# Performance work log

Hardware: AMD Instinct MI355X
Metric: run time of the kernel (lower is better)

The kernel has to match this reference:

```python
import jax, jax.numpy as jnp
import numpy as np

N_EMBD = 768

def setup_inputs() -> dict:
    key = jax.random.key(0)
    k1, k2, k3, k4 = jax.random.split(key, 4)
    B, T, head_size = 16, 1024, 128
    x = jax.random.normal(k1, (B, T, N_EMBD), dtype=jnp.float32)
    # nn.Linear(in, out, bias=False): weight stored as (out, in); we store transposed (in, out)
    s = 1.0 / np.sqrt(N_EMBD)
    Wk = jax.random.uniform(k2, (N_EMBD, head_size), jnp.float32, -s, s)
    Wq = jax.random.uniform(k3, (N_EMBD, head_size), jnp.float32, -s, s)
    Wv = jax.random.uniform(k4, (N_EMBD, head_size), jnp.float32, -s, s)
    return {"x": x, "Wk": Wk, "Wq": Wq, "Wv": Wv}

def reference(x, Wk, Wq, Wv):
    B, T, C = x.shape  # C == n_embd == 768
    k = jnp.einsum('btc,ch->bth', x, Wk)
    q = jnp.einsum('btc,ch->bth', x, Wq)
    v = jnp.einsum('btc,ch->bth', x, Wv)
    # NOTE: original scales by C**-0.5 with C = n_embd (768), not head_size.
    wei = jnp.einsum('bth,bsh->bts', q, k) * (C ** -0.5)  # (B, T, T)
    causal = jnp.tril(jnp.ones((T, T), dtype=bool))
    wei = jnp.where(causal, wei, -jnp.inf)
    wei = jax.nn.softmax(wei, axis=-1)
    # dropout p=0.0 -> identity
    return jnp.einsum('bts,bsh->bth', wei, v)
```

## Files before the change

### kernel.cpp

```cpp
#include <hip/hip_runtime.h>
#include <hip/hip_bf16.h>
#include <math.h>

#define NTOK   16384
#define NEMBD  768
#define HDIM   128

typedef __attribute__((ext_vector_type(8)))  short short8;
typedef __attribute__((ext_vector_type(16))) float floatx16;

#define MFMA32(a,b,c) __builtin_amdgcn_mfma_f32_32x32x16_bf16(a,b,c,0,0,0)

__device__ __forceinline__ unsigned short f2bf(float f) {
    unsigned u = __float_as_uint(f);
    u += 0x7fff + ((u >> 16) & 1);
    return (unsigned short)(u >> 16);
}
__device__ __forceinline__ unsigned pack2(float a, float b) {
    __hip_bfloat162 h2 = __float22bfloat162_rn(make_float2(a, b));
    union { __hip_bfloat162 h; unsigned u; } c; c.h = h2;
    return c.u;
}
__device__ __forceinline__ unsigned pack2_trunc(float a, float b) {
    return __builtin_amdgcn_perm(__float_as_uint(b), __float_as_uint(a),
                                 0x07060302u);
}

__global__ __launch_bounds__(256) void prep_w(
    const float* __restrict__ Wk, const float* __restrict__ Wq,
    const float* __restrict__ Wv, unsigned short* __restrict__ wt)
{
    __shared__ float T[64 * 65];

    const int tid = threadIdx.x;
    const int bw  = blockIdx.x / 24;
    const int rem = blockIdx.x % 24;
    const int ct  = rem >> 1, dh = rem & 1;
    const int c0  = ct * 64;
    const float* W = (bw == 0) ? Wk : ((bw == 1) ? Wq : Wv);
    const float scale = (bw == 1)
        ? (0.03608439182435161f * 1.4426950408889634f) : 1.0f;

    #pragma unroll
    for (int pass = 0; pass < 4; ++pass) {
        int idx = pass * 256 + tid;
        int c  = idx >> 4;
        int d4 = idx & 15;
        float4 v = ((const float4*)W)[(size_t)(c0 + c) * 32 + dh * 16 + d4];
        v.x *= scale; v.y *= scale; v.z *= scale; v.w *= scale;
        T[(d4 * 4 + 0) * 65 + c] = v.x;
        T[(d4 * 4 + 1) * 65 + c] = v.y;
        T[(d4 * 4 + 2) * 65 + c] = v.z;
        T[(d4 * 4 + 3) * 65 + c] = v.w;
    }
    __syncthreads();

    #pragma unroll
    for (int pass = 0; pass < 2; ++pass) {
        int idx  = pass * 256 + tid;
        int dloc = idx >> 3;
        int c8   = idx & 7;
        const float* row = &T[dloc * 65 + c8 * 8];
        uint4 u = make_uint4(pack2(row[0], row[1]), pack2(row[2], row[3]),
                             pack2(row[4], row[5]), pack2(row[6], row[7]));
        int kc    = ct * 8 + c8;
        int ksl   = kc >> 1, hb = kc & 1;
        int dglob = dh * 64 + dloc;
        int nt    = dglob >> 5;
        int lanef = (dglob & 31) + 32 * hb;
        ((uint4*)wt)[(size_t)((bw * 4 + nt) * 48 + ksl) * 64 + lanef] = u;
    }
}

__global__ __launch_bounds__(512) void qkv_fused(
    const float* __restrict__ x, const unsigned short* __restrict__ wt,
    unsigned short* __restrict__ kb, unsigned short* __restrict__ qb,
    unsigned short* __restrict__ vT)
{
    __shared__ __align__(16) char As[2][8192];

    const int tid = threadIdx.x, w = tid >> 6, lane = tid & 63;
    const int l31 = lane & 31, h = lane >> 5;
    const int wm = w >> 2, wn = w & 3;
    const int l = blockIdx.x;
    const int low3 = l & 7, rest = l >> 3;
    const int mtile = (rest / 3) * 8 + low3;
    const int nh    = rest % 3;
    const int m0 = mtile * 64;
    const int arow = tid >> 3, ac = tid & 7;

    floatx16 acc;
    #pragma unroll
    for (int i = 0; i < 16; ++i) acc[i] = 0.f;

    const float* asrc = x + (size_t)(m0 + arow) * NEMBD + ac * 8;
    const uint4* wtfb = (const uint4*)wt
                        + (size_t)(nh * 4 + wn) * 48 * 64 + lane;

    uint4 bq[2][4];
    #pragma unroll
    for (int ks = 0; ks < 4; ++ks) bq[0][ks] = wtfb[ks * 64];
    float4 a0 = ((const float4*)asrc)[0];
    float4 a1 = ((const float4*)asrc)[1];
    {
        uint4 u0 = make_uint4(pack2(a0.x, a0.y), pack2(a0.z, a0.w),
                              pack2(a1.x, a1.y), pack2(a1.z, a1.w));
        *(uint4*)(As[0] + arow * 128 + ((ac ^ (arow & 7)) * 16)) = u0;
    }
    {
        const float4* src = (const float4*)(asrc + 64);
        a0 = src[0]; a1 = src[1];
    }
    asm volatile("s_waitcnt lgkmcnt(0)" ::: "memory");
    __builtin_amdgcn_sched_barrier(0);
    __builtin_amdgcn_s_barrier();

    #pragma unroll
    for (int it = 0; it < 12; ++it) {
        char* Acur = As[it & 1];
        char* Anxt = As[(it & 1) ^ 1];

        if (it < 11) {
            #pragma unroll
            for (int ks = 0; ks < 4; ++ks)
                bq[(it + 1) & 1][ks] = wtfb[((it + 1) * 4 + ks) * 64];
            uint4 u0 = make_uint4(pack2(a0.x, a0.y), pack2(a0.z, a0.w),
                                  pack2(a1.x, a1.y), pack2(a1.z, a1.w));
            *(uint4*)(Anxt + arow * 128 + ((ac ^ (arow & 7)) * 16)) = u0;
            if (it < 10) {
                const float4* src = (const float4*)(asrc + (it + 2) * 64);
                a0 = src[0]; a1 = src[1];
            }
        }

        const int ar = wm * 32 + l31;
        #pragma unroll
        for (int ks = 0; ks < 4; ++ks) {
            short8 af = *(const short8*)(Acur + ar * 128
                                         + (((2 * ks + h) ^ (ar & 7)) * 16));
            union { uint4 q; short8 v; } bb; bb.q = bq[it & 1][ks];
            acc = MFMA32(af, bb.v, acc);
        }

        if (it < 11) {
            asm volatile("s_waitcnt lgkmcnt(0)" ::: "memory");
            __builtin_amdgcn_sched_barrier(0);
            __builtin_amdgcn_s_barrier();
        }
    }

    const int tbase = m0 + wm * 32;
    const int n0loc = wn * 32;
    if (nh < 2) {
        unsigned short* outp = (nh == 0) ? kb : qb;
        int d = n0loc + l31;
        #pragma unroll
        for (int r = 0; r < 16; ++r) {
            int t = tbase + (r & 3) + 8 * (r >> 2) + 4 * h;
            outp[(size_t)t * HDIM + d] = f2bf(acc[r]);
        }
    } else {
        int d = n0loc + l31, b = m0 >> 10, tloc = (m0 & 1023) + wm * 32;
        #pragma unroll
        for (int g = 0; g < 4; ++g) {
            int t = tloc + 8 * g + 4 * h;
            uint2 u = make_uint2(pack2(acc[4*g+0], acc[4*g+1]),
                                 pack2(acc[4*g+2], acc[4*g+3]));
            *(uint2*)((char*)vT + (((size_t)(b * HDIM + d)) * 1024 + t) * 2) = u;
        }
    }
}

__global__ __launch_bounds__(256) void attn_mfma(
    const unsigned short* __restrict__ qb, const unsigned short* __restrict__ kb,
    const unsigned short* __restrict__ vT, float* __restrict__ out)
{
    __shared__ __align__(16) float Obuf[4 * 32 * 128];
    __shared__ float lred[128];

    const int tid = threadIdx.x, w = tid >> 6, lane = tid & 63;
    const int l31 = lane & 31, h = lane >> 5;
    const int u  = blockIdx.x & 255;
    const int b  = u & 15, p = u >> 4;
    const int qt = (blockIdx.x >> 8) ? (31 - p) : p;

    const char* kb_b = (const char*)kb + (size_t)b * (1024 * 256);
    const char* qb_b = (const char*)qb + (size_t)b * (1024 * 256);
    const char* vT_b = (const char*)vT + (size_t)b * (HDIM * 2048);

    short8 qf[8];
    {
        const char* qrow = qb_b + (size_t)(qt * 32 + l31) * 256 + h * 16;
        #pragma unroll
        for (int ks = 0; ks < 8; ++ks)
            qf[ks] = *(const short8*)(qrow + ks * 32);
    }

    floatx16 o[4];
    #pragma unroll
    for (int nt = 0; nt < 4; ++nt)
        #pragma unroll
        for (int i = 0; i < 16; ++i) o[nt][i] = 0.f;
    float l_r = 0.f;

    short8 kf[8];
    if (w <= qt) {
        const char* krow = kb_b + (size_t)(w * 32 + l31) * 256 + h * 16;
        #pragma unroll
        for (int ks = 0; ks < 8; ++ks)
            kf[ks] = *(const short8*)(krow + ks * 32);
    }

    for (int st = w; st <= qt; st += 4) {
        short8 vf[8];
        {
            const char* vrow0 = vT_b + (size_t)l31 * 2048 + (size_t)st * 64 + h * 16;
            #pragma unroll
            for (int nt = 0; nt < 4; ++nt) {
                const char* vr = vrow0 + (size_t)nt * (32 * 2048);
                vf[nt * 2 + 0] = *(const short8*)(vr + 0);
                vf[nt * 2 + 1] = *(const short8*)(vr + 32);
            }
        }
        floatx16 s;
        #pragma unroll
        for (int i = 0; i < 16; ++i) s[i] = 0.f;
        __builtin_amdgcn_s_setprio(1);
        #pragma unroll
        for (int ks = 0; ks < 8; ++ks) s = MFMA32(kf[ks], qf[ks], s);
        __builtin_amdgcn_s_setprio(0);

        if (st + 4 <= qt) {
            const char* krow = kb_b + (size_t)((st + 4) * 32 + l31) * 256 + h * 16;
            #pragma unroll
            for (int ks = 0; ks < 8; ++ks)
                kf[ks] = *(const short8*)(krow + ks * 32);
        }

        if (st == qt) {
            #pragma unroll
            for (int r = 0; r < 16; ++r) {
                int key = (r & 3) + 8 * (r >> 2) + 4 * h;
                if (key > l31) s[r] = -1e30f;
            }
        }
        float p16[16];
        float ps0 = 0.f, ps1 = 0.f, ps2 = 0.f, ps3 = 0.f;
        #pragma unroll
        for (int r = 0; r < 4; ++r) {
            p16[4*r+0] = __builtin_amdgcn_exp2f(s[4*r+0]);
            p16[4*r+1] = __builtin_amdgcn_exp2f(s[4*r+1]);
            p16[4*r+2] = __builtin_amdgcn_exp2f(s[4*r+2]);
            p16[4*r+3] = __builtin_amdgcn_exp2f(s[4*r+3]);
            ps0 += p16[4*r+0]; ps1 += p16[4*r+1];
            ps2 += p16[4*r+2]; ps3 += p16[4*r+3];
        }
        l_r += (ps0 + ps1) + (ps2 + ps3);

        unsigned own[8];
        #pragma unroll
        for (int i = 0; i < 8; ++i) own[i] = pack2_trunc(p16[2*i], p16[2*i+1]);
        asm("v_permlane32_swap_b32 %0, %1" : "+v"(own[0]), "+v"(own[2]));
        asm("v_permlane32_swap_b32 %0, %1" : "+v"(own[1]), "+v"(own[3]));
        asm("v_permlane32_swap_b32 %0, %1" : "+v"(own[4]), "+v"(own[6]));
        asm("v_permlane32_swap_b32 %0, %1" : "+v"(own[5]), "+v"(own[7]));
        short8 pf[2];
        {
            union { short8 v; unsigned uu[4]; } f0, f1;
            f0.uu[0]=own[0]; f0.uu[1]=own[1]; f0.uu[2]=own[2]; f0.uu[3]=own[3];
            f1.uu[0]=own[4]; f1.uu[1]=own[5]; f1.uu[2]=own[6]; f1.uu[3]=own[7];
            pf[0] = f0.v; pf[1] = f1.v;
        }
        __builtin_amdgcn_s_setprio(1);
        #pragma unroll
        for (int nt = 0; nt < 4; ++nt) {
            o[nt] = MFMA32(vf[nt * 2 + 0], pf[0], o[nt]);
            o[nt] = MFMA32(vf[nt * 2 + 1], pf[1], o[nt]);
        }
        __builtin_amdgcn_s_setprio(0);
    }

    l_r += __shfl_xor(l_r, 32, 64);
    if (lane < 32) lred[w * 32 + l31] = l_r;
    {
        float* mybuf = &Obuf[w * 4096];
        #pragma unroll
        for (int nt = 0; nt < 4; ++nt) {
            #pragma unroll
            for (int g = 0; g < 4; ++g) {
                int chunk = nt * 8 + 2 * g + h;
                int slot  = (chunk & 24) | ((chunk & 7) ^ (l31 & 7));
                *((float4*)&mybuf[l31 * 128] + slot) =
                    make_float4(o[nt][4*g+0], o[nt][4*g+1],
                                o[nt][4*g+2], o[nt][4*g+3]);
            }
        }
    }
    __syncthreads();
    {
        int q  = tid >> 3;
        int cb = (tid & 7) * 4;
        float inv = 1.f / (lred[q] + lred[32 + q] + lred[64 + q] + lred[96 + q]);
        #pragma unroll
        for (int cc = 0; cc < 4; ++cc) {
            int chunk = cb + cc;
            int slot  = (chunk & 24) | ((chunk & 7) ^ (q & 7));
            float4 v0 = *((float4*)&Obuf[0 * 4096 + q * 128] + slot);
            float4 v1 = *((float4*)&Obuf[1 * 4096 + q * 128] + slot);
            float4 v2 = *((float4*)&Obuf[2 * 4096 + q * 128] + slot);
            float4 v3 = *((float4*)&Obuf[3 * 4096 + q * 128] + slot);
            float4 v = make_float4((v0.x + v1.x + v2.x + v3.x) * inv,
                                   (v0.y + v1.y + v2.y + v3.y) * inv,
                                   (v0.z + v1.z + v2.z + v3.z) * inv,
                                   (v0.w + v1.w + v2.w + v3.w) * inv);
            *(float4*)&out[((size_t)(b * 1024 + qt * 32 + q)) * HDIM + chunk * 4] = v;
        }
    }
}

extern "C" void kernel_launch(void* const* d_in, const int* in_sizes, int n_in,
                              void* d_out, int out_size, void* d_ws, size_t ws_size,
                              hipStream_t stream)
{
    const float* x  = (const float*)d_in[0];
    const float* Wk = (const float*)d_in[1];
    const float* Wq = (const float*)d_in[2];
    const float* Wv = (const float*)d_in[3];
    float* outp = (float*)d_out;

    char* ws = (char*)d_ws;
    unsigned short* wt = (unsigned short*)(ws);
    unsigned short* kb = (unsigned short*)(ws + 589824);
    unsigned short* qb = (unsigned short*)(ws + 4784128);
    unsigned short* vT = (unsigned short*)(ws + 8978432);

    prep_w<<<72, 256, 0, stream>>>(Wk, Wq, Wv, wt);
    qkv_fused<<<768, 512, 0, stream>>>(x, wt, kb, qb, vT);
    attn_mfma<<<512, 256, 0, stream>>>(qb, kb, vT, outp);
}
```

Measured before the change: 128.0 us.

## Split attention key tiles across eight waves per block with two-pass LDS reduction

The attention kernel now launches 512 threads (8 waves) per query tile instead of 4, so each wave strides over key tiles by 8 and the per-wave serial loop gets shorter. The cross-wave output reduction is done in two halves of the head dimension so the 64 KB LDS buffer still fits, at the cost of extra barriers. This targets latency on the long causal rows, but adds reduction work and raises register pressure under the larger launch bound.

```diff
diff --git a/kernel.cpp b/kernel.cpp
--- a/kernel.cpp
+++ b/kernel.cpp
@@ -171,12 +171,12 @@
     }
 }
 
-__global__ __launch_bounds__(256) void attn_mfma(
+__global__ __launch_bounds__(512) void attn_mfma(
     const unsigned short* __restrict__ qb, const unsigned short* __restrict__ kb,
     const unsigned short* __restrict__ vT, float* __restrict__ out)
 {
-    __shared__ __align__(16) float Obuf[4 * 32 * 128];
-    __shared__ float lred[128];
+    __shared__ __align__(16) float Obuf[8 * 32 * 64];
+    __shared__ float lred[256];
 
     const int tid = threadIdx.x, w = tid >> 6, lane = tid & 63;
     const int l31 = lane & 31, h = lane >> 5;
@@ -211,7 +211,7 @@
             kf[ks] = *(const short8*)(krow + ks * 32);
     }
 
-    for (int st = w; st <= qt; st += 4) {
+    for (int st = w; st <= qt; st += 8) {
         short8 vf[8];
         {
             const char* vrow0 = vT_b + (size_t)l31 * 2048 + (size_t)st * 64 + h * 16;
@@ -230,8 +230,8 @@
         for (int ks = 0; ks < 8; ++ks) s = MFMA32(kf[ks], qf[ks], s);
         __builtin_amdgcn_s_setprio(0);
 
-        if (st + 4 <= qt) {
-            const char* krow = kb_b + (size_t)((st + 4) * 32 + l31) * 256 + h * 16;
+        if (st + 8 <= qt) {
+            const char* krow = kb_b + (size_t)((st + 8) * 32 + l31) * 256 + h * 16;
             #pragma unroll
             for (int ks = 0; ks < 8; ++ks)
                 kf[ks] = *(const short8*)(krow + ks * 32);
@@ -282,39 +282,65 @@
 
     l_r += __shfl_xor(l_r, 32, 64);
     if (lane < 32) lred[w * 32 + l31] = l_r;
-    {
-        float* mybuf = &Obuf[w * 4096];
-        #pragma unroll
-        for (int nt = 0; nt < 4; ++nt) {
+
+    const int q  = tid >> 4;
+    const int c4 = tid & 15;
+    const int rslot = (c4 & 8) | ((c4 & 7) ^ (q & 7));
+    float inv;
+
+    {
+        float* mybuf = &Obuf[w * 2048];
+        #pragma unroll
+        for (int ntp = 0; ntp < 2; ++ntp) {
             #pragma unroll
             for (int g = 0; g < 4; ++g) {
-                int chunk = nt * 8 + 2 * g + h;
-                int slot  = (chunk & 24) | ((chunk & 7) ^ (l31 & 7));
-                *((float4*)&mybuf[l31 * 128] + slot) =
-                    make_float4(o[nt][4*g+0], o[nt][4*g+1],
-                                o[nt][4*g+2], o[nt][4*g+3]);
+                int chunk = ntp * 8 + 2 * g + h;
+                int slot  = (chunk & 8) | ((chunk & 7) ^ (l31 & 7));
+                *((float4*)&mybuf[l31 * 64] + slot) =
+                    make_float4(o[ntp][4*g+0], o[ntp][4*g+1],
+                                o[ntp][4*g+2], o[ntp][4*g+3]);
             }
         }
     }
     __syncthreads();
     {
-        int q  = tid >> 3;
-        int cb = (tid & 7) * 4;
-        float inv = 1.f / (lred[q] + lred[32 + q] + lred[64 + q] + lred[96 + q]);
-        #pragma unroll
-        for (int cc = 0; cc < 4; ++cc) {
-            int chunk = cb + cc;
-            int slot  = (chunk & 24) | ((chunk & 7) ^ (q & 7));
-            float4 v0 = *((float4*)&Obuf[0 * 4096 + q * 128] + slot);
-            float4 v1 = *((float4*)&Obuf[1 * 4096 + q * 128] + slot);
-            float4 v2 = *((float4*)&Obuf[2 * 4096 + q * 128] + slot);
-            float4 v3 = *((float4*)&Obuf[3 * 4096 + q * 128] + slot);
-            float4 v = make_float4((v0.x + v1.x + v2.x + v3.x) * inv,
-                                   (v0.y + v1.y + v2.y + v3.y) * inv,
-                                   (v0.z + v1.z + v2.z + v3.z) * inv,
-                                   (v0.w + v1.w + v2.w + v3.w) * inv);
-            *(float4*)&out[((size_t)(b * 1024 + qt * 32 + q)) * HDIM + chunk * 4] = v;
-        }
+        inv = 1.f / (((lred[q]       + lred[32 + q]) + (lred[64 + q] + lred[96 + q]))
+                   + ((lred[128 + q] + lred[160 + q]) + (lred[192 + q] + lred[224 + q])));
+        float4 a = make_float4(0.f, 0.f, 0.f, 0.f);
+        #pragma unroll
+        for (int w8 = 0; w8 < 8; ++w8) {
+            float4 v = *((float4*)&Obuf[w8 * 2048 + q * 64] + rslot);
+            a.x += v.x; a.y += v.y; a.z += v.z; a.w += v.w;
+        }
+        a.x *= inv; a.y *= inv; a.z *= inv; a.w *= inv;
+        *(float4*)&out[((size_t)(b * 1024 + qt * 32 + q)) * HDIM + c4 * 4] = a;
+    }
+    __syncthreads();
+
+    {
+        float* mybuf = &Obuf[w * 2048];
+        #pragma unroll
+        for (int ntp = 0; ntp < 2; ++ntp) {
+            #pragma unroll
+            for (int g = 0; g < 4; ++g) {
+                int chunk = ntp * 8 + 2 * g + h;
+                int slot  = (chunk & 8) | ((chunk & 7) ^ (l31 & 7));
+                *((float4*)&mybuf[l31 * 64] + slot) =
+                    make_float4(o[2 + ntp][4*g+0], o[2 + ntp][4*g+1],
+                                o[2 + ntp][4*g+2], o[2 + ntp][4*g+3]);
+            }
+        }
+    }
+    __syncthreads();
+    {
+        float4 a = make_float4(0.f, 0.f, 0.f, 0.f);
+        #pragma unroll
+        for (int w8 = 0; w8 < 8; ++w8) {
+            float4 v = *((float4*)&Obuf[w8 * 2048 + q * 64] + rslot);
+            a.x += v.x; a.y += v.y; a.z += v.z; a.w += v.w;
+        }
+        a.x *= inv; a.y *= inv; a.z *= inv; a.w *= inv;
+        *(float4*)&out[((size_t)(b * 1024 + qt * 32 + q)) * HDIM + 64 + c4 * 4] = a;
     }
 }
 
@@ -336,5 +362,5 @@
 
     prep_w<<<72, 256, 0, stream>>>(Wk, Wq, Wv, wt);
     qkv_fused<<<768, 512, 0, stream>>>(x, wt, kb, qb, vT);
-    attn_mfma<<<512, 256, 0, stream>>>(qb, kb, vT, outp);
-}
+    attn_mfma<<<512, 512, 0, stream>>>(qb, kb, vT, outp);
+}
```

Result: slower. 132.3 us (+3.4%).

## Store Q/K/V in MFMA-fragment-native layout for fully coalesced 16-byte accesses

Applied to the files above, without the earlier changes.

The projection kernel now writes K, Q and V^T directly in the per-lane fragment order the attention kernel's MFMA operands expect. It transposes the MFMA for K/Q and uses permlane32 swaps so each lane emits two 16-byte stores. The attention kernel then loads each fragment as a contiguous lane-indexed uint4, replacing strided row loads. The aim is fewer, fully coalesced global transactions in both kernels, at the cost of coupling the intermediate layout tightly to the MFMA fragment mapping.

```diff
diff --git a/kernel.cpp b/kernel.cpp
--- a/kernel.cpp
+++ b/kernel.cpp
@@ -139,7 +139,8 @@
             short8 af = *(const short8*)(Acur + ar * 128
                                          + (((2 * ks + h) ^ (ar & 7)) * 16));
             union { uint4 q; short8 v; } bb; bb.q = bq[it & 1][ks];
-            acc = MFMA32(af, bb.v, acc);
+            if (nh < 2) acc = MFMA32(bb.v, af, acc);
+            else        acc = MFMA32(af, bb.v, acc);
         }
 
         if (it < 11) {
@@ -149,25 +150,27 @@
         }
     }
 
-    const int tbase = m0 + wm * 32;
-    const int n0loc = wn * 32;
+    const int bidx = m0 >> 10;
+    const int ktl  = ((m0 & 1023) >> 5) + wm;
+    unsigned own[8];
+    #pragma unroll
+    for (int i = 0; i < 8; ++i) own[i] = pack2(acc[2*i], acc[2*i+1]);
+    asm("v_permlane32_swap_b32 %0, %1" : "+v"(own[0]), "+v"(own[2]));
+    asm("v_permlane32_swap_b32 %0, %1" : "+v"(own[1]), "+v"(own[3]));
+    asm("v_permlane32_swap_b32 %0, %1" : "+v"(own[4]), "+v"(own[6]));
+    asm("v_permlane32_swap_b32 %0, %1" : "+v"(own[5]), "+v"(own[7]));
+    uint4 u1 = make_uint4(own[0], own[1], own[2], own[3]);
+    uint4 u2 = make_uint4(own[4], own[5], own[6], own[7]);
     if (nh < 2) {
-        unsigned short* outp = (nh == 0) ? kb : qb;
-        int d = n0loc + l31;
-        #pragma unroll
-        for (int r = 0; r < 16; ++r) {
-            int t = tbase + (r & 3) + 8 * (r >> 2) + 4 * h;
-            outp[(size_t)t * HDIM + d] = f2bf(acc[r]);
-        }
+        uint4* outp = (uint4*)((nh == 0) ? kb : qb);
+        size_t base = ((size_t)(bidx * 32 + ktl) * 8 + 2 * wn) * 64 + lane;
+        outp[base]      = u1;
+        outp[base + 64] = u2;
     } else {
-        int d = n0loc + l31, b = m0 >> 10, tloc = (m0 & 1023) + wm * 32;
-        #pragma unroll
-        for (int g = 0; g < 4; ++g) {
-            int t = tloc + 8 * g + 4 * h;
-            uint2 u = make_uint2(pack2(acc[4*g+0], acc[4*g+1]),
-                                 pack2(acc[4*g+2], acc[4*g+3]));
-            *(uint2*)((char*)vT + (((size_t)(b * HDIM + d)) * 1024 + t) * 2) = u;
-        }
+        uint4* outp = (uint4*)vT;
+        size_t base = ((size_t)(bidx * 32 + ktl) * 4 + wn) * 2 * 64 + lane;
+        outp[base]      = u1;
+        outp[base + 64] = u2;
     }
 }
 
@@ -184,17 +187,14 @@
     const int b  = u & 15, p = u >> 4;
     const int qt = (blockIdx.x >> 8) ? (31 - p) : p;
 
-    const char* kb_b = (const char*)kb + (size_t)b * (1024 * 256);
-    const char* qb_b = (const char*)qb + (size_t)b * (1024 * 256);
-    const char* vT_b = (const char*)vT + (size_t)b * (HDIM * 2048);
+    const uint4* qbu = (const uint4*)qb + (size_t)b * 16384 + lane;
+    const uint4* kbu = (const uint4*)kb + (size_t)b * 16384 + lane;
+    const uint4* vtu = (const uint4*)vT + (size_t)b * 16384 + lane;
 
     short8 qf[8];
-    {
-        const char* qrow = qb_b + (size_t)(qt * 32 + l31) * 256 + h * 16;
-        #pragma unroll
-        for (int ks = 0; ks < 8; ++ks)
-            qf[ks] = *(const short8*)(qrow + ks * 32);
-    }
+    #pragma unroll
+    for (int ks = 0; ks < 8; ++ks)
+        qf[ks] = *(const short8*)(qbu + ((size_t)qt * 8 + ks) * 64);
 
     floatx16 o[4];
     #pragma unroll
@@ -205,22 +205,17 @@
 
     short8 kf[8];
     if (w <= qt) {
-        const char* krow = kb_b + (size_t)(w * 32 + l31) * 256 + h * 16;
         #pragma unroll
         for (int ks = 0; ks < 8; ++ks)
-            kf[ks] = *(const short8*)(krow + ks * 32);
+            kf[ks] = *(const short8*)(kbu + ((size_t)w * 8 + ks) * 64);
     }
 
     for (int st = w; st <= qt; st += 4) {
         short8 vf[8];
-        {
-            const char* vrow0 = vT_b + (size_t)l31 * 2048 + (size_t)st * 64 + h * 16;
-            #pragma unroll
-            for (int nt = 0; nt < 4; ++nt) {
-                const char* vr = vrow0 + (size_t)nt * (32 * 2048);
-                vf[nt * 2 + 0] = *(const short8*)(vr + 0);
-                vf[nt * 2 + 1] = *(const short8*)(vr + 32);
-            }
+        #pragma unroll
+        for (int nt = 0; nt < 4; ++nt) {
+            vf[nt * 2 + 0] = *(const short8*)(vtu + (((size_t)st * 4 + nt) * 2 + 0) * 64);
+            vf[nt * 2 + 1] = *(const short8*)(vtu + (((size_t)st * 4 + nt) * 2 + 1) * 64);
         }
         floatx16 s;
         #pragma unroll
@@ -231,10 +226,9 @@
         __builtin_amdgcn_s_setprio(0);
 
         if (st + 4 <= qt) {
-            const char* krow = kb_b + (size_t)((st + 4) * 32 + l31) * 256 + h * 16;
             #pragma unroll
             for (int ks = 0; ks < 8; ++ks)
-                kf[ks] = *(const short8*)(krow + ks * 32);
+                kf[ks] = *(const short8*)(kbu + ((size_t)(st + 4) * 8 + ks) * 64);
         }
 
         if (st == qt) {
```

After: 118.8 us. -7.2%, faster.
